# Optimization experiments

Hardware: AMD Instinct MI355X
Metric: run time of the kernel (lower is better)

Reference implementation:

```python
import jax, jax.numpy as jnp
import numpy as np

LEARNING_RATE = 0.01


def setup_inputs() -> dict:
    key = jax.random.key(0)
    k1, k2 = jax.random.split(key)
    O, D = 512, 128  # output_dim, input_dim; batch must equal output_dim for the broadcast
    x = jax.random.normal(k1, (O, D), dtype=jnp.float32)
    weights = jax.random.normal(k2, (O, O, D), dtype=jnp.float32)
    return {"x": x, "weights": weights}


def reference(x, weights):
    # x: (B, D) with B == O; weights: (O, O, D)
    O = weights.shape[0]
    sigma = O / 2.0
    x = x.reshape(-1, weights.shape[-1])
    diff = weights - x[:, None, :]                      # (O, O, D)
    distances = jnp.sum(diff * diff, axis=-1)            # (O, O)
    winner = jnp.argmin(distances, axis=1)               # (O,)
    neighborhood = jnp.exp(-distances / (2.0 * sigma ** 2))  # (O, O)
    delta = LEARNING_RATE * neighborhood[..., None] * (x[:, None, :] - weights)  # (O, O, D)
    # torch: self.weights.data += torch.sum(delta, dim=0)  -> (O, D) broadcast over rows
    new_weights = weights + jnp.sum(delta, axis=0)        # (O, O, D)
    return winner, new_weights
```

## Files before the change

### kernel.cpp

```cpp
#include <hip/hip_runtime.h>
#include <stdint.h>

#define O_DIM 512
#define D_DIM 128
#define LR 0.01f
#define INV2SIG2 7.62939453125e-6f

typedef float f32x4 __attribute__((ext_vector_type(4)));


__global__ __launch_bounds__(256) void som_pass1(
    const float* __restrict__ X,
    const float* __restrict__ W,
    float* __restrict__ dist,
    float* __restrict__ Spart)
{
    const int j     = blockIdx.x >> 2;
    const int chunk = blockIdx.x & 3;
    const int wave  = threadIdx.x >> 6;
    const int lane  = threadIdx.x & 63;
    const int g     = lane >> 4;
    const int i16   = lane & 15;
    const int dA    = i16 * 4;
    const int dB    = 64 + dA;

    float acc[8];
    #pragma unroll
    for (int u = 0; u < 8; ++u) acc[u] = 0.f;

    const int bbase = chunk * 128 + wave * 32 + g;

    #pragma unroll 2
    for (int k = 0; k < 8; ++k) {
        const int b = bbase + k * 4;
        const float* wrow = W + ((size_t)b * O_DIM + j) * D_DIM;
        const float* xrow = X + (size_t)b * D_DIM;
        const float4 wa = *(const float4*)(wrow + dA);
        const float4 wb = *(const float4*)(wrow + dB);
        const float4 xa = *(const float4*)(xrow + dA);
        const float4 xb = *(const float4*)(xrow + dB);

        float dx[8];
        dx[0] = wa.x - xa.x; dx[1] = wa.y - xa.y;
        dx[2] = wa.z - xa.z; dx[3] = wa.w - xa.w;
        dx[4] = wb.x - xb.x; dx[5] = wb.y - xb.y;
        dx[6] = wb.z - xb.z; dx[7] = wb.w - xb.w;

        float s = 0.f;
        #pragma unroll
        for (int u = 0; u < 8; ++u) s = fmaf(dx[u], dx[u], s);
        s += __shfl_xor(s, 1, 64);
        s += __shfl_xor(s, 2, 64);
        s += __shfl_xor(s, 4, 64);
        s += __shfl_xor(s, 8, 64);

        if (i16 == 0) dist[(size_t)b * O_DIM + j] = s;

        const float c = LR * __expf(-s * INV2SIG2);
        #pragma unroll
        for (int u = 0; u < 8; ++u) acc[u] = fmaf(-c, dx[u], acc[u]);
    }

    #pragma unroll
    for (int u = 0; u < 8; ++u) {
        acc[u] += __shfl_xor(acc[u], 16, 64);
        acc[u] += __shfl_xor(acc[u], 32, 64);
    }

    __shared__ float sacc[4][D_DIM];
    if (g == 0) {
        #pragma unroll
        for (int u = 0; u < 4; ++u) {
            sacc[wave][dA + u] = acc[u];
            sacc[wave][dB + u] = acc[4 + u];
        }
    }
    __syncthreads();
    if (threadIdx.x < D_DIM) {
        const int d = threadIdx.x;
        Spart[((size_t)chunk * O_DIM + j) * D_DIM + d] =
            sacc[0][d] + sacc[1][d] + sacc[2][d] + sacc[3][d];
    }
}

__global__ __launch_bounds__(256) void som_pass2(
    const float* __restrict__ W,
    const float* __restrict__ dist,
    const float* __restrict__ Spart,
    float* __restrict__ out)
{
    const int jt = blockIdx.x >> 5;
    const int ic = blockIdx.x & 31;
    const int t  = threadIdx.x;
    float* __restrict__ outW = out + O_DIM;

    if (blockIdx.x < O_DIM && t < 64) {
        const int b = blockIdx.x;
        unsigned long long best = ~0ull;
        #pragma unroll
        for (int k = 0; k < 8; ++k) {
            const int jj = k * 64 + t;
            const float s = dist[(size_t)b * O_DIM + jj];
            const unsigned long long key =
                ((unsigned long long)__float_as_uint(s) << 32) | (unsigned int)jj;
            best = key < best ? key : best;
        }
        #pragma unroll
        for (int m = 32; m >= 1; m >>= 1) {
            const unsigned long long o = __shfl_xor(best, m, 64);
            best = o < best ? o : best;
        }
        if (t == 0) out[b] = (float)(unsigned int)(best & 0xFFFFFFFFull);
    }

    const size_t SPLANE = (size_t)O_DIM * D_DIM;
    const size_t soff = (size_t)jt * 8 * D_DIM + (size_t)t * 4;
    const f32x4 s0 = *(const f32x4*)(Spart + soff);
    const f32x4 s1 = *(const f32x4*)(Spart + SPLANE + soff);
    const f32x4 s2 = *(const f32x4*)(Spart + 2 * SPLANE + soff);
    const f32x4 s3 = *(const f32x4*)(Spart + 3 * SPLANE + soff);
    const f32x4 s4 = s0 + s1 + s2 + s3;

    const size_t base = (size_t)(ic * 16) * O_DIM * D_DIM + soff;
    #pragma unroll 4
    for (int i = 0; i < 16; ++i) {
        const size_t e = base + (size_t)i * O_DIM * D_DIM;
        const f32x4 w4 = *(const f32x4*)(W + e);
        __builtin_nontemporal_store(w4 + s4, (f32x4*)(outW + e));
    }
}


__global__ __launch_bounds__(256) void som_pass1_atomic(
    const float* __restrict__ X, const float* __restrict__ W,
    float* __restrict__ S, unsigned long long* __restrict__ wkey)
{
    const int j = blockIdx.x >> 2, chunk = blockIdx.x & 3;
    const int wave = threadIdx.x >> 6, lane = threadIdx.x & 63;
    const int d0 = lane * 2;
    float accx = 0.f, accy = 0.f;
    const int b_end = chunk * 128 + 128;
    for (int b = chunk * 128 + wave; b < b_end; b += 4) {
        const float2 w2 = *(const float2*)(W + ((size_t)b * O_DIM + j) * D_DIM + d0);
        const float2 x2 = *(const float2*)(X + (size_t)b * D_DIM + d0);
        const float dx = w2.x - x2.x, dy = w2.y - x2.y;
        float s = dx * dx + dy * dy;
        #pragma unroll
        for (int m = 32; m >= 1; m >>= 1) s += __shfl_xor(s, m, 64);
        if (lane == 0)
            atomicMin(&wkey[b], ((unsigned long long)__float_as_uint(s) << 32) | (unsigned)j);
        const float c = LR * __expf(-s * INV2SIG2);
        accx -= c * dx; accy -= c * dy;
    }
    __shared__ float sacc[D_DIM];
    if (threadIdx.x < D_DIM) sacc[threadIdx.x] = 0.f;
    __syncthreads();
    atomicAdd(&sacc[d0], accx); atomicAdd(&sacc[d0 + 1], accy);
    __syncthreads();
    if (threadIdx.x < D_DIM) atomicAdd(&S[(size_t)j * D_DIM + threadIdx.x], sacc[threadIdx.x]);
}

__global__ __launch_bounds__(256) void som_pass2_atomic(
    const float* __restrict__ W, const float* __restrict__ S,
    const unsigned long long* __restrict__ wkey, float* __restrict__ out)
{
    const size_t tid = (size_t)blockIdx.x * blockDim.x + threadIdx.x;
    if (tid < O_DIM) out[tid] = (float)(unsigned int)(wkey[tid] & 0xFFFFFFFFull);
    float* __restrict__ outW = out + O_DIM;
    const size_t total4 = (size_t)O_DIM * O_DIM * D_DIM / 4;
    const size_t stride = (size_t)gridDim.x * blockDim.x;
    for (size_t i = tid; i < total4; i += stride) {
        const size_t e = i * 4;
        const float4 w4 = *(const float4*)(W + e);
        const float4 s4 = *(const float4*)(S + (e & (size_t)(O_DIM * D_DIM - 1)));
        float4 o4 = {w4.x + s4.x, w4.y + s4.y, w4.z + s4.z, w4.w + s4.w};
        *(float4*)(outW + e) = o4;
    }
}

extern "C" void kernel_launch(void* const* d_in, const int* in_sizes, int n_in,
                              void* d_out, int out_size, void* d_ws, size_t ws_size,
                              hipStream_t stream)
{
    const float* X = (const float*)d_in[0];
    const float* W = (const float*)d_in[1];
    float* out = (float*)d_out;

    const size_t DIST_BYTES  = (size_t)O_DIM * O_DIM * sizeof(float);
    const size_t SPART_BYTES = 4ull * O_DIM * D_DIM * sizeof(float);

    if (ws_size >= DIST_BYTES + SPART_BYTES) {
        float* dist  = (float*)d_ws;
        float* Spart = (float*)((char*)d_ws + DIST_BYTES);
        som_pass1<<<dim3(2048), dim3(256), 0, stream>>>(X, W, dist, Spart);
        som_pass2<<<dim3(2048), dim3(256), 0, stream>>>(W, dist, Spart, out);
    } else {
        float* S = (float*)d_ws;
        unsigned long long* wkey =
            (unsigned long long*)((char*)d_ws + (size_t)O_DIM * D_DIM * sizeof(float));
        hipMemsetAsync(S, 0, (size_t)O_DIM * D_DIM * sizeof(float), stream);
        hipMemsetAsync(wkey, 0xFF, (size_t)O_DIM * sizeof(unsigned long long), stream);
        som_pass1_atomic<<<dim3(2048), dim3(256), 0, stream>>>(X, W, S, wkey);
        som_pass2_atomic<<<dim3(2048), dim3(256), 0, stream>>>(W, S, wkey, out);
    }
}
```

Baseline: 66.52 us.

## Fuse distance reduction and weight update into one kernel per output column

Merges the reduction and the update passes so each block owns one column j, computes its 512 distances and the summed delta, then immediately re-reads that column's weights (likely still in L2/MALL) to write the updated output. The partial-sum buffer and its extra global round trip go away, and a small separate kernel does the argmin. The main loop is also restructured to issue four rows of loads before computing, raising memory-level parallelism. The trade-off is a smaller grid (512 blocks instead of 2048), which may reduce occupancy on a 256-CU device, and the second read of W depends on cache hits.

New measurement: 65.58 us. About the same (-1.4%).

```diff
diff --git a/kernel.cpp b/kernel.cpp
--- a/kernel.cpp
+++ b/kernel.cpp
@@ -8,57 +8,62 @@
 
 typedef float f32x4 __attribute__((ext_vector_type(4)));
 
-
-__global__ __launch_bounds__(256) void som_pass1(
+__global__ __launch_bounds__(256) void som_fused(
     const float* __restrict__ X,
     const float* __restrict__ W,
     float* __restrict__ dist,
-    float* __restrict__ Spart)
+    float* __restrict__ outW)
 {
-    const int j     = blockIdx.x >> 2;
-    const int chunk = blockIdx.x & 3;
-    const int wave  = threadIdx.x >> 6;
-    const int lane  = threadIdx.x & 63;
-    const int g     = lane >> 4;
-    const int i16   = lane & 15;
-    const int dA    = i16 * 4;
-    const int dB    = 64 + dA;
+    const int j    = blockIdx.x;
+    const int wave = threadIdx.x >> 6;
+    const int lane = threadIdx.x & 63;
+    const int g    = lane >> 4;
+    const int i16  = lane & 15;
+    const int dA   = i16 * 4;
+    const int dB   = 64 + dA;
 
     float acc[8];
     #pragma unroll
     for (int u = 0; u < 8; ++u) acc[u] = 0.f;
 
-    const int bbase = chunk * 128 + wave * 32 + g;
+    const int bbase = wave * 4 + g;
 
     #pragma unroll 2
-    for (int k = 0; k < 8; ++k) {
-        const int b = bbase + k * 4;
-        const float* wrow = W + ((size_t)b * O_DIM + j) * D_DIM;
-        const float* xrow = X + (size_t)b * D_DIM;
-        const float4 wa = *(const float4*)(wrow + dA);
-        const float4 wb = *(const float4*)(wrow + dB);
-        const float4 xa = *(const float4*)(xrow + dA);
-        const float4 xb = *(const float4*)(xrow + dB);
+    for (int k = 0; k < 32; k += 4) {
+        float4 wa[4], wb[4], xa[4], xb[4];
+        int bb[4];
+        #pragma unroll
+        for (int u = 0; u < 4; ++u) {
+            bb[u] = bbase + (k + u) * 16;
+            const float* wrow = W + ((size_t)bb[u] * O_DIM + j) * D_DIM;
+            const float* xrow = X + (size_t)bb[u] * D_DIM;
+            wa[u] = *(const float4*)(wrow + dA);
+            wb[u] = *(const float4*)(wrow + dB);
+            xa[u] = *(const float4*)(xrow + dA);
+            xb[u] = *(const float4*)(xrow + dB);
+        }
+        #pragma unroll
+        for (int u = 0; u < 4; ++u) {
+            float dx[8];
+            dx[0] = wa[u].x - xa[u].x; dx[1] = wa[u].y - xa[u].y;
+            dx[2] = wa[u].z - xa[u].z; dx[3] = wa[u].w - xa[u].w;
+            dx[4] = wb[u].x - xb[u].x; dx[5] = wb[u].y - xb[u].y;
+            dx[6] = wb[u].z - xb[u].z; dx[7] = wb[u].w - xb[u].w;
 
-        float dx[8];
-        dx[0] = wa.x - xa.x; dx[1] = wa.y - xa.y;
-        dx[2] = wa.z - xa.z; dx[3] = wa.w - xa.w;
-        dx[4] = wb.x - xb.x; dx[5] = wb.y - xb.y;
-        dx[6] = wb.z - xb.z; dx[7] = wb.w - xb.w;
+            float s = 0.f;
+            #pragma unroll
+            for (int v = 0; v < 8; ++v) s = fmaf(dx[v], dx[v], s);
+            s += __shfl_xor(s, 1, 64);
+            s += __shfl_xor(s, 2, 64);
+            s += __shfl_xor(s, 4, 64);
+            s += __shfl_xor(s, 8, 64);
 
-        float s = 0.f;
-        #pragma unroll
-        for (int u = 0; u < 8; ++u) s = fmaf(dx[u], dx[u], s);
-        s += __shfl_xor(s, 1, 64);
-        s += __shfl_xor(s, 2, 64);
-        s += __shfl_xor(s, 4, 64);
-        s += __shfl_xor(s, 8, 64);
+            if (i16 == 0) dist[(size_t)bb[u] * O_DIM + j] = s;
 
-        if (i16 == 0) dist[(size_t)b * O_DIM + j] = s;
-
-        const float c = LR * __expf(-s * INV2SIG2);
-        #pragma unroll
-        for (int u = 0; u < 8; ++u) acc[u] = fmaf(-c, dx[u], acc[u]);
+            const float c = LR * __expf(-s * INV2SIG2);
+            #pragma unroll
+            for (int v = 0; v < 8; ++v) acc[v] = fmaf(-c, dx[v], acc[v]);
+        }
     }
 
     #pragma unroll
@@ -68,6 +73,7 @@
     }
 
     __shared__ float sacc[4][D_DIM];
+    __shared__ float sS[D_DIM];
     if (g == 0) {
         #pragma unroll
         for (int u = 0; u < 4; ++u) {
@@ -78,56 +84,45 @@
     __syncthreads();
     if (threadIdx.x < D_DIM) {
         const int d = threadIdx.x;
-        Spart[((size_t)chunk * O_DIM + j) * D_DIM + d] =
-            sacc[0][d] + sacc[1][d] + sacc[2][d] + sacc[3][d];
+        sS[d] = sacc[0][d] + sacc[1][d] + sacc[2][d] + sacc[3][d];
+    }
+    __syncthreads();
+
+    const f32x4 sA = *(const f32x4*)(sS + dA);
+    const f32x4 sB = *(const f32x4*)(sS + dB);
+
+    #pragma unroll 4
+    for (int k = 0; k < 32; ++k) {
+        const int b = bbase + k * 16;
+        const size_t e = ((size_t)b * O_DIM + j) * D_DIM;
+        const f32x4 w4a = *(const f32x4*)(W + e + dA);
+        const f32x4 w4b = *(const f32x4*)(W + e + dB);
+        __builtin_nontemporal_store(w4a + sA, (f32x4*)(outW + e + dA));
+        __builtin_nontemporal_store(w4b + sB, (f32x4*)(outW + e + dB));
     }
 }
 
-__global__ __launch_bounds__(256) void som_pass2(
-    const float* __restrict__ W,
+__global__ __launch_bounds__(64) void som_argmin(
     const float* __restrict__ dist,
-    const float* __restrict__ Spart,
     float* __restrict__ out)
 {
-    const int jt = blockIdx.x >> 5;
-    const int ic = blockIdx.x & 31;
-    const int t  = threadIdx.x;
-    float* __restrict__ outW = out + O_DIM;
-
-    if (blockIdx.x < O_DIM && t < 64) {
-        const int b = blockIdx.x;
-        unsigned long long best = ~0ull;
-        #pragma unroll
-        for (int k = 0; k < 8; ++k) {
-            const int jj = k * 64 + t;
-            const float s = dist[(size_t)b * O_DIM + jj];
-            const unsigned long long key =
-                ((unsigned long long)__float_as_uint(s) << 32) | (unsigned int)jj;
-            best = key < best ? key : best;
-        }
-        #pragma unroll
-        for (int m = 32; m >= 1; m >>= 1) {
-            const unsigned long long o = __shfl_xor(best, m, 64);
-            best = o < best ? o : best;
-        }
-        if (t == 0) out[b] = (float)(unsigned int)(best & 0xFFFFFFFFull);
+    const int b = blockIdx.x;
+    const int lane = threadIdx.x;
+    unsigned long long best = ~0ull;
+    #pragma unroll
+    for (int k = 0; k < 8; ++k) {
+        const int jj = k * 64 + lane;
+        const float s = dist[(size_t)b * O_DIM + jj];
+        const unsigned long long key =
+            ((unsigned long long)__float_as_uint(s) << 32) | (unsigned int)jj;
+        best = key < best ? key : best;
     }
-
-    const size_t SPLANE = (size_t)O_DIM * D_DIM;
-    const size_t soff = (size_t)jt * 8 * D_DIM + (size_t)t * 4;
-    const f32x4 s0 = *(const f32x4*)(Spart + soff);
-    const f32x4 s1 = *(const f32x4*)(Spart + SPLANE + soff);
-    const f32x4 s2 = *(const f32x4*)(Spart + 2 * SPLANE + soff);
-    const f32x4 s3 = *(const f32x4*)(Spart + 3 * SPLANE + soff);
-    const f32x4 s4 = s0 + s1 + s2 + s3;
-
-    const size_t base = (size_t)(ic * 16) * O_DIM * D_DIM + soff;
-    #pragma unroll 4
-    for (int i = 0; i < 16; ++i) {
-        const size_t e = base + (size_t)i * O_DIM * D_DIM;
-        const f32x4 w4 = *(const f32x4*)(W + e);
-        __builtin_nontemporal_store(w4 + s4, (f32x4*)(outW + e));
+    #pragma unroll
+    for (int m = 32; m >= 1; m >>= 1) {
+        const unsigned long long o = __shfl_xor(best, m, 64);
+        best = o < best ? o : best;
     }
+    if (lane == 0) out[b] = (float)(unsigned int)(best & 0xFFFFFFFFull);
 }
 
 
@@ -186,14 +181,12 @@
     const float* W = (const float*)d_in[1];
     float* out = (float*)d_out;
 
-    const size_t DIST_BYTES  = (size_t)O_DIM * O_DIM * sizeof(float);
-    const size_t SPART_BYTES = 4ull * O_DIM * D_DIM * sizeof(float);
+    const size_t DIST_BYTES = (size_t)O_DIM * O_DIM * sizeof(float);
 
-    if (ws_size >= DIST_BYTES + SPART_BYTES) {
-        float* dist  = (float*)d_ws;
-        float* Spart = (float*)((char*)d_ws + DIST_BYTES);
-        som_pass1<<<dim3(2048), dim3(256), 0, stream>>>(X, W, dist, Spart);
-        som_pass2<<<dim3(2048), dim3(256), 0, stream>>>(W, dist, Spart, out);
+    if (ws_size >= DIST_BYTES) {
+        float* dist = (float*)d_ws;
+        som_fused <<<dim3(512), dim3(256), 0, stream>>>(X, W, dist, out + O_DIM);
+        som_argmin<<<dim3(512), dim3(64),  0, stream>>>(dist, out);
     } else {
         float* S = (float*)d_ws;
         unsigned long long* wkey =
```
